# Optimization experiments

Measured on AMD Instinct MI355X. Metric: run time of the kernel, lower is better.

Reference implementation:

```python
import jax, jax.numpy as jnp
import numpy as np
from jax import lax

SCALES = (1.0, 3.0, 7.0)
EPS = 1e-8

SOBEL_X = jnp.asarray(np.array([[-1,0,1],[-2,0,2],[-1,0,1]], np.float32))
SOBEL_Y = jnp.asarray(np.array([[-1,-2,-1],[0,0,0],[1,2,1]], np.float32))

def _gauss_deriv_kernel(sigma):
    k = int(6 * sigma + 1)
    if k % 2 == 0:
        k += 1
    x = np.arange(k, dtype=np.float32) - k // 2
    ker = -x / sigma ** 3 * np.exp(-x ** 2 / (2 * sigma ** 2))
    ker = ker / np.abs(ker).sum()
    return jnp.asarray(ker)  # (k,)

SPECTRAL_KERNELS = [_gauss_deriv_kernel(s) for s in SCALES]

def _conv2d_1ch(x, k):
    # x: (B,1,H,W), k: (3,3) -> cross-correlation, padding=1
    return lax.conv_general_dilated(x, k[None, None], (1, 1), [(1, 1), (1, 1)],
                                    dimension_numbers=('NCHW', 'OIHW', 'NCHW'))

def _spectral_conv(x_r, k):
    # x_r: (N,1,C), k: (ks,) -> conv1d along C, padding ks//2
    p = k.shape[0] // 2
    return lax.conv_general_dilated(x_r, k[None, None, :], (1,), [(p, p)],
                                    dimension_numbers=('NCH', 'OIH', 'NCH'))

def setup_inputs() -> dict:
    key = jax.random.key(0)
    ks = jax.random.split(key, 5)
    B, C, H, W = 8, 128, 128, 128
    return {
        'x': jax.random.normal(ks[0], (B, C, H, W), jnp.float32),
        'meta_features': jax.random.normal(ks[1], (B, 12), jnp.float32),
        'w1': jax.random.normal(ks[2], (24, 12), jnp.float32) * 0.2,
        'b1': jnp.zeros((24,), jnp.float32),
        'w2': jax.random.normal(ks[3], (12, 24), jnp.float32) * 0.2,
        'b2': jnp.zeros((12,), jnp.float32),
    }

def reference(x, meta_features, w1, b1, w2, b2):
    B, C, H, W = x.shape
    # weight MLP (eval mode: dropout is identity)
    h = jax.nn.relu(meta_features @ w1.T + b1)
    weights = jax.nn.sigmoid(h @ w2.T + b2)          # (B,12)
    alpha = weights[:, 0][:, None, None, None]
    beta = weights[:, 1][:, None, None, None]
    gamma = weights[:, 2][:, None, None, None]

    # spatial gradient: sobel on band-mean image
    x_mean = x.mean(axis=1, keepdims=True)            # (B,1,H,W)
    gx = _conv2d_1ch(x_mean, SOBEL_X)
    gy = _conv2d_1ch(x_mean, SOBEL_Y)
    spatial_grad = jnp.sqrt(gx ** 2 + gy ** 2 + EPS)  # (B,1,H,W)

    # spectral gradient: multi-scale gaussian derivative along C
    x_r = x.transpose(0, 2, 3, 1).reshape(-1, 1, C)   # (B*H*W,1,C)
    scale_outs = []
    for k in SPECTRAL_KERNELS:
        g = jnp.abs(_spectral_conv(x_r, k)).mean(axis=2)   # (B*H*W,1)
        scale_outs.append(g.reshape(B, H, W)[:, None])     # (B,1,H,W)
    spectral_grad = jnp.max(jnp.stack(scale_outs, axis=0), axis=0)

    # mixed gradient: sobel of medium-scale spectral derivative volume
    vol = jnp.abs(_spectral_conv(x_r, SPECTRAL_KERNELS[1]))  # (B*H*W,1,C)
    vol = vol.reshape(B, H, W, C).transpose(0, 3, 1, 2)      # (B,C,H,W)
    kx = jnp.tile(SOBEL_X[None, None], (C, 1, 1, 1))         # (C,1,3,3) depthwise
    ky = jnp.tile(SOBEL_Y[None, None], (C, 1, 1, 1))
    mx = lax.conv_general_dilated(vol, kx, (1, 1), [(1, 1), (1, 1)],
                                  feature_group_count=C,
                                  dimension_numbers=('NCHW', 'OIHW', 'NCHW'))
    my = lax.conv_general_dilated(vol, ky, (1, 1), [(1, 1), (1, 1)],
                                  feature_group_count=C,
                                  dimension_numbers=('NCHW', 'OIHW', 'NCHW'))
    mixed_grad = jnp.sqrt(mx ** 2 + my ** 2 + EPS).mean(axis=1, keepdims=True)

    return jnp.sqrt(alpha * spatial_grad ** 2 + beta * spectral_grad ** 2
                    + gamma * mixed_grad ** 2 + EPS)
```

## Files before the change

kernel.cpp:

```cpp
#include <hip/hip_runtime.h>
#include <math.h>

#define BB 8
#define CC 128
#define HH 128
#define WW 128
#define HWs (HH * WW)

#define TH 8
#define TW 8
#define NCX 10
#define NCOL 100

#define K7 7
#define K19 19
#define K43 43

#define XPAD 24
#define CSX 184
#define CSV 168
#define VSUB 40

struct Kers { float k7[K7]; float k19[K19]; float k43[K43]; };

__device__ __forceinline__ ushort f2bf(float f) {
    uint u = __float_as_uint(f);
    u += 0x7FFFu + ((u >> 16) & 1u);
    return (ushort)(u >> 16);
}
__device__ __forceinline__ float bflo(uint u) { return __uint_as_float(u << 16); }
__device__ __forceinline__ float bfhi(uint u) { return __uint_as_float(u & 0xFFFF0000u); }

__global__ void __launch_bounds__(256, 2) holo_kernel(
        const float* __restrict__ x, const float* __restrict__ meta,
        const float* __restrict__ w1, const float* __restrict__ b1,
        const float* __restrict__ w2, const float* __restrict__ b2,
        float* __restrict__ out, Kers kers) {
    __shared__ __align__(16) ushort xs[NCOL * CSX];
    __shared__ __align__(16) ushort vol[NCOL * CSV];
    __shared__ float mimg[NCOL];
    __shared__ float hbuf[24];
    __shared__ float abg[3];

    const int tid = threadIdx.x;
    const int wg  = blockIdx.x;
    const int swz = (wg & 7) * 256 + (wg >> 3);
    const int b   = swz >> 8;
    const int rem = swz & 255;
    const int h0  = (rem >> 4) * TH;
    const int w0  = (rem & 15) * TW;

    if (tid < 24) {
        float s = b1[tid];
        #pragma unroll
        for (int i = 0; i < 12; ++i) s = fmaf(meta[b * 12 + i], w1[tid * 12 + i], s);
        hbuf[tid] = fmaxf(s, 0.0f);
    }

    const float* xb = x + (size_t)b * (CC * HWs);
    for (int idx = tid; idx < NCOL * 46; idx += 256) {
        const int q  = idx % NCOL;
        const int s4 = idx / NCOL;
        uint lo = 0, hi = 0;
        if (s4 >= 6 && s4 < 38) {
            const int c  = 4 * s4 - XPAD;
            const int hh = h0 - 1 + q / NCX, ww = w0 - 1 + q % NCX;
            if ((unsigned)hh < HH && (unsigned)ww < WW) {
                const float* gp = xb + (size_t)c * HWs + hh * WW + ww;
                lo = (uint)f2bf(gp[0])       | ((uint)f2bf(gp[HWs])     << 16);
                hi = (uint)f2bf(gp[2 * HWs]) | ((uint)f2bf(gp[3 * HWs]) << 16);
            }
        }
        *(uint2*)(xs + q * CSX + 4 * s4) = make_uint2(lo, hi);
    }
    __syncthreads();

    if (tid < 3) {
        float s = b2[tid];
        #pragma unroll
        for (int j = 0; j < 24; ++j) s = fmaf(hbuf[j], w2[tid * 24 + j], s);
        abg[tid] = 1.0f / (1.0f + expf(-s));
    }

    for (int it = tid; it < NCOL * 4; it += 256) {
        const int q = it % NCOL, k = it / NCOL;
        const uint4* wp = (const uint4*)(xs + q * CSX + 8 + 32 * k);
        float f2[64];
        #pragma unroll
        for (int t = 0; t < 8; ++t) {
            uint4 u = wp[t];
            f2[8*t+0]=bflo(u.x); f2[8*t+1]=bfhi(u.x); f2[8*t+2]=bflo(u.y); f2[8*t+3]=bfhi(u.y);
            f2[8*t+4]=bflo(u.z); f2[8*t+5]=bfhi(u.z); f2[8*t+6]=bflo(u.w); f2[8*t+7]=bfhi(u.w);
        }
        uint ov[16];
        #pragma unroll
        for (int m = 0; m < 32; ++m) {
            float s = 0.0f;
            #pragma unroll
            for (int j = 0; j < K19; ++j) s = fmaf(kers.k19[j], f2[m + 7 + j], s);
            const ushort hv = f2bf(fabsf(s));
            if ((m & 1) == 0) ov[m >> 1] = hv; else ov[m >> 1] |= (uint)hv << 16;
        }
        uint4* vp = (uint4*)(vol + q * CSV + VSUB * k);
        vp[0] = make_uint4(ov[0],  ov[1],  ov[2],  ov[3]);
        vp[1] = make_uint4(ov[4],  ov[5],  ov[6],  ov[7]);
        vp[2] = make_uint4(ov[8],  ov[9],  ov[10], ov[11]);
        vp[3] = make_uint4(ov[12], ov[13], ov[14], ov[15]);
    }
    if (tid >= 156) {
        const int col = tid - 156;
        const uint4* cp = (const uint4*)(xs + col * CSX + XPAD);
        float s = 0.0f;
        #pragma unroll
        for (int t = 0; t < 16; ++t) {
            uint4 u = cp[t];
            s += bflo(u.x) + bfhi(u.x) + bflo(u.y) + bfhi(u.y)
               + bflo(u.z) + bfhi(u.z) + bflo(u.w) + bfhi(u.w);
        }
        mimg[col] = s * (1.0f / CC);
    }
    __syncthreads();

    const int p = tid >> 2, sub = tid & 3;
    const int py = p >> 3, px = p & 7;
    const int q  = (py + 1) * NCX + (px + 1);

    float g1 = 0.0f, g3 = 0.0f;
    {
        float f[80];
        const uint4* ap = (const uint4*)(xs + q * CSX + 32 * sub);
        #pragma unroll
        for (int t = 0; t < 10; ++t) {
            uint4 u = ap[t];
            f[8*t+0]=bflo(u.x); f[8*t+1]=bfhi(u.x); f[8*t+2]=bflo(u.y); f[8*t+3]=bfhi(u.y);
            f[8*t+4]=bflo(u.z); f[8*t+5]=bfhi(u.z); f[8*t+6]=bflo(u.w); f[8*t+7]=bfhi(u.w);
        }
        #pragma unroll
        for (int m = 0; m < 32; ++m) {
            float s43 = 0.0f;
            #pragma unroll
            for (int j = 0; j < K43; ++j) s43 = fmaf(kers.k43[j], f[m + 3 + j], s43);
            float s7 = 0.0f;
            #pragma unroll
            for (int j = 0; j < K7; ++j) s7 = fmaf(kers.k7[j], f[m + 21 + j], s7);
            g3 += fabsf(s43);
            g1 += fabsf(s7);
        }
    }
    float g2 = 0.0f, macc = 0.0f;
    const int nq[9] = { q-11, q-10, q-9, q-1, q, q+1, q+9, q+10, q+11 };
    #pragma unroll
    for (int ss = 0; ss < 4; ++ss) {
        uint4 u[9];
        #pragma unroll
        for (int n = 0; n < 9; ++n)
            u[n] = *(const uint4*)(vol + nq[n] * CSV + sub * VSUB + 8 * ss);
        #pragma unroll
        for (int t = 0; t < 8; ++t) {
            float v[9];
            #pragma unroll
            for (int n = 0; n < 9; ++n) {
                const uint w = (t & 4) ? ((t & 2) ? u[n].w : u[n].z)
                                       : ((t & 2) ? u[n].y : u[n].x);
                v[n] = (t & 1) ? bfhi(w) : bflo(w);
            }
            g2 += v[4];
            const float mx = (v[2] - v[0]) + 2.0f * (v[5] - v[3]) + (v[8] - v[6]);
            const float my = (v[6] - v[0]) + 2.0f * (v[7] - v[1]) + (v[8] - v[2]);
            macc += sqrtf(mx * mx + my * my + 1e-8f);
        }
    }
    g1   += __shfl_xor(g1, 1);   g1   += __shfl_xor(g1, 2);
    g2   += __shfl_xor(g2, 1);   g2   += __shfl_xor(g2, 2);
    g3   += __shfl_xor(g3, 1);   g3   += __shfl_xor(g3, 2);
    macc += __shfl_xor(macc, 1); macc += __shfl_xor(macc, 2);

    if (sub == 0) {
        const float spec = fmaxf(fmaxf(g1, g2), g3) * (1.0f / CC);
        const float mix  = macc * (1.0f / CC);
        const float m_mm = mimg[q-11], m_m0 = mimg[q-10], m_mp = mimg[q-9];
        const float m_0m = mimg[q-1],                      m_0p = mimg[q+1];
        const float m_pm = mimg[q+9],  m_p0 = mimg[q+10],  m_pp = mimg[q+11];
        const float gx = (m_mp - m_mm) + 2.0f * (m_0p - m_0m) + (m_pp - m_pm);
        const float gy = (m_pm - m_mm) + 2.0f * (m_p0 - m_m0) + (m_pp - m_mp);
        const float sg2 = gx * gx + gy * gy + 1e-8f;
        const float al = abg[0], be = abg[1], ga = abg[2];
        const float o = sqrtf(al * sg2 + be * spec * spec + ga * mix * mix + 1e-8f);
        out[((size_t)b * HH + (h0 + py)) * WW + (w0 + px)] = o;
    }
}

static void make_ker(float sigma, int k, float* outk) {
    int half = k / 2;
    float asum = 0.0f;
    for (int i = 0; i < k; ++i) {
        float xx = (float)(i - half);
        float v = -xx / (sigma * sigma * sigma) * expf(-xx * xx / (2.0f * sigma * sigma));
        outk[i] = v;
        asum += fabsf(v);
    }
    for (int i = 0; i < k; ++i) outk[i] /= asum;
}

extern "C" void kernel_launch(void* const* d_in, const int* in_sizes, int n_in,
                              void* d_out, int out_size, void* d_ws, size_t ws_size,
                              hipStream_t stream) {
    const float* x    = (const float*)d_in[0];
    const float* meta = (const float*)d_in[1];
    const float* w1   = (const float*)d_in[2];
    const float* b1   = (const float*)d_in[3];
    const float* w2   = (const float*)d_in[4];
    const float* b2   = (const float*)d_in[5];
    float* outp = (float*)d_out;

    Kers kers;
    make_ker(1.0f, K7,  kers.k7);
    make_ker(3.0f, K19, kers.k19);
    make_ker(7.0f, K43, kers.k43);

    holo_kernel<<<BB * 16 * 16, 256, 0, stream>>>(x, meta, w1, b1, w2, b2, outp, kers);
}
```

Measured before the change: 188.0 us.

## Split fused kernel into volume and gradient kernels with global intermediate

Replaces the single fused kernel, which recomputed the spectral derivative volume over a 10x10 halo tile, with two kernels. The first computes the bf16 derivative volume, the band-mean image and the MLP weights into workspace. The second reads neighbour volumes from global memory for the Sobel step. It also rewrites the 1D convolutions in scatter form over registers, and raises the occupancy target from 2 to 4 blocks. This removes halo recomputation and shrinks shared memory, but adds a 32MB intermediate written and read through global memory, a second launch, and staging x twice.

```diff
diff --git a/kernel.cpp b/kernel.cpp
--- a/kernel.cpp
+++ b/kernel.cpp
@@ -9,6 +9,7 @@
 
 #define TH 8
 #define TW 8
+#define NP 64
 #define NCX 10
 #define NCOL 100
 
@@ -30,6 +31,210 @@
 }
 __device__ __forceinline__ float bflo(uint u) { return __uint_as_float(u << 16); }
 __device__ __forceinline__ float bfhi(uint u) { return __uint_as_float(u & 0xFFFF0000u); }
+
+__device__ __forceinline__ void stage_tile(const float* __restrict__ xb,
+                                           ushort* __restrict__ xs,
+                                           int tid, int h0, int w0) {
+    for (int idx = tid; idx < NP * 46; idx += 256) {
+        const int q  = idx & 63;
+        const int s4 = idx >> 6;
+        uint lo = 0, hi = 0;
+        if (s4 >= 6 && s4 < 38) {
+            const int c  = 4 * s4 - XPAD;
+            const int hh = h0 + (q >> 3), ww = w0 + (q & 7);
+            const float* gp = xb + (size_t)c * HWs + hh * WW + ww;
+            lo = (uint)f2bf(gp[0])       | ((uint)f2bf(gp[HWs])     << 16);
+            hi = (uint)f2bf(gp[2 * HWs]) | ((uint)f2bf(gp[3 * HWs]) << 16);
+        }
+        *(uint2*)(xs + q * CSX + 4 * s4) = make_uint2(lo, hi);
+    }
+}
+
+__global__ void __launch_bounds__(256, 4) vol_kernel(
+        const float* __restrict__ x, const float* __restrict__ meta,
+        const float* __restrict__ w1, const float* __restrict__ b1,
+        const float* __restrict__ w2, const float* __restrict__ b2,
+        ushort* __restrict__ volg, float* __restrict__ mimgg,
+        float* __restrict__ abgg, Kers kers) {
+    __shared__ __align__(16) ushort xs[NP * CSX];
+    __shared__ float hbuf[192];
+
+    const int tid = threadIdx.x;
+    const int wg  = blockIdx.x;
+    const int swz = (wg & 7) * 256 + (wg >> 3);
+    const int b   = swz >> 8;
+    const int rem = swz & 255;
+    const int h0  = (rem >> 4) * TH, w0 = (rem & 15) * TW;
+
+    if (wg == 0 && tid < 192) {
+        const int bb = tid / 24, j = tid - bb * 24;
+        float s = b1[j];
+        #pragma unroll
+        for (int i = 0; i < 12; ++i) s = fmaf(meta[bb * 12 + i], w1[j * 12 + i], s);
+        hbuf[tid] = fmaxf(s, 0.0f);
+    }
+    stage_tile(x + (size_t)b * CC * HWs, xs, tid, h0, w0);
+    __syncthreads();
+    if (wg == 0 && tid < 24) {
+        const int bb = tid / 3, o = tid - bb * 3;
+        float s = b2[o];
+        #pragma unroll
+        for (int j = 0; j < 24; ++j) s = fmaf(hbuf[bb * 24 + j], w2[o * 24 + j], s);
+        abgg[tid] = 1.0f / (1.0f + expf(-s));
+    }
+
+    const int q = tid & 63, k = tid >> 6;
+    const int hh = h0 + (q >> 3), ww = w0 + (q & 7);
+    const size_t pixg = ((size_t)b * HH + hh) * WW + ww;
+    {
+        float acc[32];
+        #pragma unroll
+        for (int m = 0; m < 32; ++m) acc[m] = 0.0f;
+        const uint4* wp = (const uint4*)(xs + q * CSX + 32 * k + 8);
+        #pragma unroll
+        for (int t = 0; t < 8; ++t) {
+            const uint4 u = wp[t];
+            float w8[8];
+            w8[0]=bflo(u.x); w8[1]=bfhi(u.x); w8[2]=bflo(u.y); w8[3]=bfhi(u.y);
+            w8[4]=bflo(u.z); w8[5]=bfhi(u.z); w8[6]=bflo(u.w); w8[7]=bfhi(u.w);
+            #pragma unroll
+            for (int e = 0; e < 8; ++e) {
+                const int i = 8 * t + e;
+                #pragma unroll
+                for (int m = 0; m < 32; ++m) {
+                    const int j = i - m - 7;
+                    if (j >= 0 && j < K19) acc[m] = fmaf(kers.k19[j], w8[e], acc[m]);
+                }
+            }
+        }
+        uint ov[16];
+        #pragma unroll
+        for (int m = 0; m < 32; ++m) {
+            const ushort hv = f2bf(fabsf(acc[m]));
+            if ((m & 1) == 0) ov[m >> 1] = hv; else ov[m >> 1] |= (uint)hv << 16;
+        }
+        uint4* vp = (uint4*)(volg + pixg * CC + 32 * k);
+        vp[0] = make_uint4(ov[0],  ov[1],  ov[2],  ov[3]);
+        vp[1] = make_uint4(ov[4],  ov[5],  ov[6],  ov[7]);
+        vp[2] = make_uint4(ov[8],  ov[9],  ov[10], ov[11]);
+        vp[3] = make_uint4(ov[12], ov[13], ov[14], ov[15]);
+    }
+    if (tid < NP) {
+        const uint4* cp = (const uint4*)(xs + tid * CSX + XPAD);
+        float s = 0.0f;
+        #pragma unroll
+        for (int t = 0; t < 16; ++t) {
+            const uint4 u = cp[t];
+            s += bflo(u.x) + bfhi(u.x) + bflo(u.y) + bfhi(u.y)
+               + bflo(u.z) + bfhi(u.z) + bflo(u.w) + bfhi(u.w);
+        }
+        const int hh2 = h0 + (tid >> 3), ww2 = w0 + (tid & 7);
+        mimgg[((size_t)b * HH + hh2) * WW + ww2] = s * (1.0f / CC);
+    }
+}
+
+__global__ void __launch_bounds__(256, 4) grad_kernel(
+        const float* __restrict__ x, const ushort* __restrict__ volg,
+        const float* __restrict__ mimgg, const float* __restrict__ abgg,
+        float* __restrict__ out, Kers kers) {
+    __shared__ __align__(16) ushort xs[NP * CSX];
+
+    const int tid = threadIdx.x;
+    const int wg  = blockIdx.x;
+    const int swz = (wg & 7) * 256 + (wg >> 3);
+    const int b   = swz >> 8;
+    const int rem = swz & 255;
+    const int h0  = (rem >> 4) * TH, w0 = (rem & 15) * TW;
+
+    stage_tile(x + (size_t)b * CC * HWs, xs, tid, h0, w0);
+    __syncthreads();
+
+    const int p = tid >> 2, sub = tid & 3;
+    const int py = p >> 3, px = p & 7;
+    const int h = h0 + py, w = w0 + px;
+    const size_t pixg = ((size_t)b * HH + h) * WW + w;
+
+    float a43[32], a7[32];
+    #pragma unroll
+    for (int m = 0; m < 32; ++m) { a43[m] = 0.0f; a7[m] = 0.0f; }
+    {
+        const uint4* ap = (const uint4*)(xs + p * CSX + 32 * sub);
+        #pragma unroll
+        for (int t = 0; t < 10; ++t) {
+            const uint4 u = ap[t];
+            float w8[8];
+            w8[0]=bflo(u.x); w8[1]=bfhi(u.x); w8[2]=bflo(u.y); w8[3]=bfhi(u.y);
+            w8[4]=bflo(u.z); w8[5]=bfhi(u.z); w8[6]=bflo(u.w); w8[7]=bfhi(u.w);
+            #pragma unroll
+            for (int e = 0; e < 8; ++e) {
+                const int i = 8 * t + e;
+                #pragma unroll
+                for (int m = 0; m < 32; ++m) {
+                    const int j43 = i - m - 3;
+                    if (j43 >= 0 && j43 < K43) a43[m] = fmaf(kers.k43[j43], w8[e], a43[m]);
+                    const int j7 = i - m - 21;
+                    if (j7 >= 0 && j7 < K7)    a7[m]  = fmaf(kers.k7[j7],  w8[e], a7[m]);
+                }
+            }
+        }
+    }
+    float g1 = 0.0f, g3 = 0.0f;
+    #pragma unroll
+    for (int m = 0; m < 32; ++m) { g1 += fabsf(a7[m]); g3 += fabsf(a43[m]); }
+
+    bool vld[9];
+    const ushort* vb[9];
+    #pragma unroll
+    for (int n = 0; n < 9; ++n) {
+        const int dy = n / 3 - 1, dx = n % 3 - 1;
+        const int hn = h + dy, wn = w + dx;
+        vld[n] = ((unsigned)hn < HH) && ((unsigned)wn < WW);
+        const size_t pn = vld[n] ? (pixg + dy * WW + dx) : pixg;
+        vb[n] = volg + pn * CC + 32 * sub;
+    }
+    float g2 = 0.0f, macc = 0.0f;
+    #pragma unroll
+    for (int ss = 0; ss < 4; ++ss) {
+        uint4 u[9];
+        #pragma unroll
+        for (int n = 0; n < 9; ++n)
+            u[n] = vld[n] ? *(const uint4*)(vb[n] + 8 * ss) : make_uint4(0, 0, 0, 0);
+        #pragma unroll
+        for (int t = 0; t < 8; ++t) {
+            float v[9];
+            #pragma unroll
+            for (int n = 0; n < 9; ++n) {
+                const uint wsel = (t & 4) ? ((t & 2) ? u[n].w : u[n].z)
+                                          : ((t & 2) ? u[n].y : u[n].x);
+                v[n] = (t & 1) ? bfhi(wsel) : bflo(wsel);
+            }
+            g2 += v[4];
+            const float mx = (v[2] - v[0]) + 2.0f * (v[5] - v[3]) + (v[8] - v[6]);
+            const float my = (v[6] - v[0]) + 2.0f * (v[7] - v[1]) + (v[8] - v[2]);
+            macc += sqrtf(mx * mx + my * my + 1e-8f);
+        }
+    }
+    g1   += __shfl_xor(g1, 1);   g1   += __shfl_xor(g1, 2);
+    g2   += __shfl_xor(g2, 1);   g2   += __shfl_xor(g2, 2);
+    g3   += __shfl_xor(g3, 1);   g3   += __shfl_xor(g3, 2);
+    macc += __shfl_xor(macc, 1); macc += __shfl_xor(macc, 2);
+
+    if (sub == 0) {
+        const float spec = fmaxf(fmaxf(g1, g2), g3) * (1.0f / CC);
+        const float mix  = macc * (1.0f / CC);
+        float mg[9];
+        #pragma unroll
+        for (int n = 0; n < 9; ++n) {
+            const int dy = n / 3 - 1, dx = n % 3 - 1;
+            mg[n] = vld[n] ? mimgg[pixg + dy * WW + dx] : 0.0f;
+        }
+        const float gx = (mg[2] - mg[0]) + 2.0f * (mg[5] - mg[3]) + (mg[8] - mg[6]);
+        const float gy = (mg[6] - mg[0]) + 2.0f * (mg[7] - mg[1]) + (mg[8] - mg[2]);
+        const float sg2 = gx * gx + gy * gy + 1e-8f;
+        const float al = abgg[b * 3 + 0], be = abgg[b * 3 + 1], ga = abgg[b * 3 + 2];
+        out[pixg] = sqrtf(al * sg2 + be * spec * spec + ga * mix * mix + 1e-8f);
+    }
+}
 
 __global__ void __launch_bounds__(256, 2) holo_kernel(
         const float* __restrict__ x, const float* __restrict__ meta,
@@ -56,7 +261,6 @@
         for (int i = 0; i < 12; ++i) s = fmaf(meta[b * 12 + i], w1[tid * 12 + i], s);
         hbuf[tid] = fmaxf(s, 0.0f);
     }
-
     const float* xb = x + (size_t)b * (CC * HWs);
     for (int idx = tid; idx < NCOL * 46; idx += 256) {
         const int q  = idx % NCOL;
@@ -74,14 +278,12 @@
         *(uint2*)(xs + q * CSX + 4 * s4) = make_uint2(lo, hi);
     }
     __syncthreads();
-
     if (tid < 3) {
         float s = b2[tid];
         #pragma unroll
         for (int j = 0; j < 24; ++j) s = fmaf(hbuf[j], w2[tid * 24 + j], s);
         abg[tid] = 1.0f / (1.0f + expf(-s));
     }
-
     for (int it = tid; it < NCOL * 4; it += 256) {
         const int q = it % NCOL, k = it / NCOL;
         const uint4* wp = (const uint4*)(xs + q * CSX + 8 + 32 * k);
@@ -124,7 +326,6 @@
     const int p = tid >> 2, sub = tid & 3;
     const int py = p >> 3, px = p & 7;
     const int q  = (py + 1) * NCX + (px + 1);
-
     float g1 = 0.0f, g3 = 0.0f;
     {
         float f[80];
@@ -160,9 +361,9 @@
             float v[9];
             #pragma unroll
             for (int n = 0; n < 9; ++n) {
-                const uint w = (t & 4) ? ((t & 2) ? u[n].w : u[n].z)
-                                       : ((t & 2) ? u[n].y : u[n].x);
-                v[n] = (t & 1) ? bfhi(w) : bflo(w);
+                const uint wsel = (t & 4) ? ((t & 2) ? u[n].w : u[n].z)
+                                          : ((t & 2) ? u[n].y : u[n].x);
+                v[n] = (t & 1) ? bfhi(wsel) : bflo(wsel);
             }
             g2 += v[4];
             const float mx = (v[2] - v[0]) + 2.0f * (v[5] - v[3]) + (v[8] - v[6]);
@@ -174,7 +375,6 @@
     g2   += __shfl_xor(g2, 1);   g2   += __shfl_xor(g2, 2);
     g3   += __shfl_xor(g3, 1);   g3   += __shfl_xor(g3, 2);
     macc += __shfl_xor(macc, 1); macc += __shfl_xor(macc, 2);
-
     if (sub == 0) {
         const float spec = fmaxf(fmaxf(g1, g2), g3) * (1.0f / CC);
         const float mix  = macc * (1.0f / CC);
@@ -218,5 +418,20 @@
     make_ker(3.0f, K19, kers.k19);
     make_ker(7.0f, K43, kers.k43);
 
-    holo_kernel<<<BB * 16 * 16, 256, 0, stream>>>(x, meta, w1, b1, w2, b2, outp, kers);
-}
+    const size_t VOLB  = (size_t)BB * HH * WW * CC * sizeof(ushort);
+    const size_t MIMGB = (size_t)BB * HH * WW * sizeof(float);
+    const size_t ABGB  = 24 * sizeof(float);
+
+    if (ws_size >= VOLB + MIMGB + ABGB) {
+        ushort* volg  = (ushort*)d_ws;
+        float*  mimgg = (float*)((char*)d_ws + VOLB);
+        float*  abgg  = (float*)((char*)d_ws + VOLB + MIMGB);
+        vol_kernel<<<BB * 16 * 16, 256, 0, stream>>>(x, meta, w1, b1, w2, b2,
+                                                     volg, mimgg, abgg, kers);
+        grad_kernel<<<BB * 16 * 16, 256, 0, stream>>>(x, volg, mimgg, abgg,
+                                                      outp, kers);
+    } else {
+        holo_kernel<<<BB * 16 * 16, 256, 0, stream>>>(x, meta, w1, b1, w2, b2,
+                                                      outp, kers);
+    }
+}
```

Result: slower. 218.2 us (+16.1%).
